# Kernel optimization log

Measured on AMD Instinct MI355X. Metric: run time of the kernel, lower is better.

Reference implementation:

```python
import jax, jax.numpy as jnp
from jax import lax
import numpy as np

C_IN, C_OUT, G, K, PAD = 64, 128, 4, 3, 1
P = K * K
CG = C_IN // G
N, H, W = 8, 64, 64
LN_EPS = 1e-6
BN_EPS = 1e-5


def setup_inputs() -> dict:
    key = jax.random.key(0)
    ks = jax.random.split(key, 32)
    r = lambda i, shape, s=0.05: jax.random.normal(ks[i], shape, dtype=jnp.float32) * s
    return dict(
        x=jax.random.normal(ks[0], (N, C_IN, H, W), dtype=jnp.float32),
        reflectance=jax.random.uniform(ks[1], (N, 1, H, W), dtype=jnp.float32),
        gain_w1=r(2, (C_IN, C_IN // 4)), gain_b1=r(3, (C_IN // 4,)),
        gain_w2=r(4, (C_IN // 4, C_IN)), gain_b2=r(5, (C_IN,)),
        tap_w=r(6, (C_IN,)), tap_b=r(7, (C_IN,)),
        dw_w=r(8, (K, K, 1, C_IN)), dw_b=r(9, (C_IN,)),
        ln_g=jnp.ones((C_IN,), jnp.float32), ln_b=jnp.zeros((C_IN,), jnp.float32),
        inp_w=r(10, (C_IN, C_IN)), inp_b=r(11, (C_IN,)),
        off_w=r(12, (C_IN, G * P * 2), 0.02), off_b=r(13, (G * P * 2,), 0.02),
        mask_w=r(14, (C_IN, G * P), 0.02), mask_b=r(15, (G * P,), 0.02),
        outp_w=r(16, (C_IN, C_IN)), outp_b=r(17, (C_IN,)),
        conv_w=r(18, (C_IN, C_OUT)), conv_b=r(19, (C_OUT,)),
        bn1_g=jnp.ones((C_IN,), jnp.float32), bn1_b=jnp.zeros((C_IN,), jnp.float32),
        bn1_m=r(20, (C_IN,)),
        bn1_v=jax.random.uniform(ks[21], (C_IN,), minval=0.5, maxval=1.5),
        bn2_g=jnp.ones((C_OUT,), jnp.float32), bn2_b=jnp.zeros((C_OUT,), jnp.float32),
        bn2_m=r(22, (C_OUT,)),
        bn2_v=jax.random.uniform(ks[23], (C_OUT,), minval=0.5, maxval=1.5),
    )


def _bilinear_gather(xg, py, px):
    # xg: (N, Hp, Wp, G, CG); py/px: (N, H, W, G, P) absolute pixel coords
    # replicates F.grid_sample(mode='bilinear', padding_mode='zeros', align_corners=False)
    n_, Hp, Wp = xg.shape[0], xg.shape[1], xg.shape[2]
    y0 = jnp.floor(py)
    x0 = jnp.floor(px)
    wy = py - y0
    wx = px - x0
    nI = jnp.arange(n_).reshape(n_, 1, 1, 1, 1)
    gI = jnp.arange(G).reshape(1, 1, 1, G, 1)
    out = jnp.zeros(py.shape + (CG,), xg.dtype)
    for dy in (0, 1):
        for dx in (0, 1):
            yi = y0 + dy
            xi = x0 + dx
            w = (wy if dy else 1.0 - wy) * (wx if dx else 1.0 - wx)
            valid = (yi >= 0) & (yi < Hp) & (xi >= 0) & (xi < Wp)
            yc = jnp.clip(yi, 0, Hp - 1).astype(jnp.int32)
            xc = jnp.clip(xi, 0, Wp - 1).astype(jnp.int32)
            v = xg[nI, yc, xc, gI]  # (N, H, W, G, P, CG)
            out = out + (w * valid.astype(w.dtype))[..., None] * v
    return out


def reference(x, reflectance, gain_w1, gain_b1, gain_w2, gain_b2, tap_w, tap_b,
              dw_w, dw_b, ln_g, ln_b, inp_w, inp_b, off_w, off_b, mask_w, mask_b,
              outp_w, outp_b, conv_w, conv_b, bn1_g, bn1_b, bn1_m, bn1_v,
              bn2_g, bn2_b, bn2_m, bn2_v):
    n_, c_, h_, w_ = x.shape
    # ---- GainBlock (SE-style): x * sigmoid(mlp(avgpool(x))) + x ----
    pooled = x.mean(axis=(2, 3))                               # (N, C)
    g = jax.nn.relu(pooled @ gain_w1 + gain_b1)
    gain = jax.nn.sigmoid(g @ gain_w2 + gain_b2)               # (N, C)
    x = x * gain[:, :, None, None] + x
    # ---- ReflectiveFeedback: x + relu(conv1x1(reflectance)) ----
    refl = jax.nn.relu(reflectance * tap_w[None, :, None, None] + tap_b[None, :, None, None])
    x = x + refl                                               # (N, C, H, W)
    # ---- DCNv3 (pytorch version, group=4, k=3, pad=1, stride=1) ----
    xh = jnp.transpose(x, (0, 2, 3, 1))                        # NHWC
    xp = xh @ inp_w + inp_b                                    # input_proj
    dw = lax.conv_general_dilated(xh, dw_w, (1, 1), 'SAME',
                                  feature_group_count=c_,
                                  dimension_numbers=('NHWC', 'HWIO', 'NHWC')) + dw_b
    mu = dw.mean(-1, keepdims=True)
    var = dw.var(-1, keepdims=True)
    dw = ln_g * (dw - mu) * lax.rsqrt(var + LN_EPS) + ln_b     # LN channels_last
    dw = jax.nn.gelu(dw, approximate=False)
    offset = (dw @ off_w + off_b).reshape(n_, h_, w_, G, P, 2)
    mask = jax.nn.softmax((dw @ mask_w + mask_b).reshape(n_, h_, w_, G, P), axis=-1)
    # dcnv3_core: pad input, build reference + dilation grids (normalized by padded size)
    xpad = jnp.pad(xp, ((0, 0), (PAD, PAD), (PAD, PAD), (0, 0)))
    Hp, Wp = h_ + 2 * PAD, w_ + 2 * PAD
    ctr = (K - 1) // 2  # = (dilation*(k-1))//2 with dilation=1
    ref_y = (jnp.arange(h_, dtype=jnp.float32) + ctr + 0.5) / Hp
    ref_x = (jnp.arange(w_, dtype=jnp.float32) + ctr + 0.5) / Wp
    kk = jnp.arange(K, dtype=jnp.float32) - ctr                # [-1, 0, 1]
    gx = jnp.repeat(kk, K) / Wp                                # w-outer, h-inner order
    gy = jnp.tile(kk, K) / Hp
    loc_x = (ref_x[None, None, :, None, None] + gx[None, None, None, None, :]
             + offset[..., 0] / Wp)                            # (N,H,W,G,P)
    loc_y = (ref_y[None, :, None, None, None] + gy[None, None, None, None, :]
             + offset[..., 1] / Hp)
    px = loc_x * Wp - 0.5   # align_corners=False pixel coords
    py = loc_y * Hp - 0.5
    xg = xpad.reshape(n_, Hp, Wp, G, CG)
    samp = _bilinear_gather(xg, py, px)                        # (N,H,W,G,P,CG)
    dcn = (samp * mask[..., None]).sum(axis=4).reshape(n_, h_, w_, c_)
    dcn = dcn @ outp_w + outp_b                                # output_proj
    y = jnp.transpose(dcn, (0, 3, 1, 2))                       # back to NCHW
    # ---- bn1 -> relu -> conv1x1 -> bn2 -> relu (eval-mode BN) ----
    y = bn1_g[None, :, None, None] * (y - bn1_m[None, :, None, None]) \
        * lax.rsqrt(bn1_v[None, :, None, None] + BN_EPS) + bn1_b[None, :, None, None]
    y = jax.nn.relu(y)
    y = jnp.einsum('nchw,cd->ndhw', y, conv_w) + conv_b[None, :, None, None]
    y = bn2_g[None, :, None, None] * (y - bn2_m[None, :, None, None]) \
        * lax.rsqrt(bn2_v[None, :, None, None] + BN_EPS) + bn2_b[None, :, None, None]
    return jax.nn.relu(y)
```

## Files before the change

kernel.cpp:

```cpp
#include <hip/hip_runtime.h>
#include <math.h>


__global__ __launch_bounds__(256) void k_pool(const float* x, float* pooled) {
    __shared__ float red[256];
    int b = blockIdx.x;
    int nc = ((b & 7) << 6) | (b >> 3);
    const float4* p4 = reinterpret_cast<const float4*>(x + (size_t)nc * 4096);
    float s = 0.f;
    for (int i = threadIdx.x; i < 1024; i += 256) {
        float4 v = p4[i];
        s += v.x + v.y + v.z + v.w;
    }
    red[threadIdx.x] = s;
    __syncthreads();
    for (int o = 128; o > 0; o >>= 1) {
        if (threadIdx.x < o) red[threadIdx.x] += red[threadIdx.x + o];
        __syncthreads();
    }
    if (threadIdx.x == 0) pooled[nc] = red[0] * (1.f / 4096.f);
}

__global__ __launch_bounds__(256) void k_xsproj(
        const float* x, const float* refl,
        const float* tap_w, const float* tap_b,
        const float* pooled,
        const float* gw1, const float* gb1,
        const float* gw2, const float* gb2,
        const float* inp_w, const float* inp_b,
        float* xs, float* xpad) {
    __shared__ float wl[64 * 64];
    __shared__ float tile[64 * 17];
    __shared__ float xsrow[16][68];
    __shared__ float hid[16];
    __shared__ float gain[64];
    __shared__ float rrow[16];
    int b = blockIdx.x;
    int n = b & 7, rem = b >> 3;
    int h = rem >> 2, wc = rem & 3, w0 = wc * 16;
    int nh = n * 64 + h;
    int tid = threadIdx.x;

    for (int i = tid; i < 1024; i += 256)
        *reinterpret_cast<float4*>(&wl[i * 4]) = reinterpret_cast<const float4*>(inp_w)[i];
    {
        int c = tid >> 2, wq = (tid & 3) * 4;
        const float4 v = *reinterpret_cast<const float4*>(
            &x[(((size_t)(n * 64 + c)) * 64 + h) * 64 + w0 + wq]);
        tile[c * 17 + wq + 0] = v.x;
        tile[c * 17 + wq + 1] = v.y;
        tile[c * 17 + wq + 2] = v.z;
        tile[c * 17 + wq + 3] = v.w;
    }
    if (tid < 16) rrow[tid] = refl[n * 4096 + h * 64 + w0 + tid];
    if (tid >= 64 && tid < 80) {
        int j = tid - 64;
        float s = gb1[j];
        for (int c = 0; c < 64; ++c) s += pooled[n * 64 + c] * gw1[c * 16 + j];
        hid[j] = fmaxf(s, 0.f);
    }
    __syncthreads();

    if (tid < 64) {
        float s = gb2[tid];
        #pragma unroll
        for (int j = 0; j < 16; ++j) s += hid[j] * gw2[j * 64 + tid];
        gain[tid] = 1.f + 1.f / (1.f + expf(-s));
    }
    __syncthreads();

    {
        int c = tid & 63, wbq = tid >> 6;
        float gv = gain[c], tw = tap_w[c], tb = tap_b[c];
        #pragma unroll
        for (int k = 0; k < 4; ++k) {
            int w = wbq + k * 4;
            float r = fmaxf(rrow[w] * tw + tb, 0.f);
            float v = tile[c * 17 + w] * gv + r;
            xsrow[w][c] = v;
            xs[(((size_t)nh) * 64 + w0 + w) * 64 + c] = v;
        }
    }
    __syncthreads();

    {
        int co = tid & 63, wg = tid >> 6;
        float acc[4];
        float bv = inp_b[co];
        #pragma unroll
        for (int i = 0; i < 4; ++i) acc[i] = bv;
        for (int c4 = 0; c4 < 64; c4 += 4) {
            float q0 = wl[(c4 + 0) * 64 + co];
            float q1 = wl[(c4 + 1) * 64 + co];
            float q2 = wl[(c4 + 2) * 64 + co];
            float q3 = wl[(c4 + 3) * 64 + co];
            #pragma unroll
            for (int i = 0; i < 4; ++i) {
                float4 d = *reinterpret_cast<const float4*>(&xsrow[wg * 4 + i][c4]);
                acc[i] += d.x * q0 + d.y * q1 + d.z * q2 + d.w * q3;
            }
        }
        const size_t rowb = (((size_t)n * 66) + (h + 1)) * 66;
        #pragma unroll
        for (int i = 0; i < 4; ++i) {
            int w = wg * 4 + i;
            xpad[(rowb + (w0 + w + 1)) * 64 + co] = acc[i];
        }
        if (wc == 0 && tid < 64) xpad[rowb * 64 + tid] = 0.f;
        if (wc == 3 && tid < 64) xpad[(rowb + 65) * 64 + tid] = 0.f;
        if (h == 0 || h == 63) {
            const size_t rb = (((size_t)n * 66) + (h == 0 ? 0 : 65)) * 66;
            for (int i = tid; i < 1024; i += 256) {
                int q = 1 + w0 + (i >> 6), cc = i & 63;
                xpad[(rb + q) * 64 + cc] = 0.f;
            }
            if (wc == 0 && tid < 64) xpad[rb * 64 + tid] = 0.f;
            if (wc == 3 && tid < 64) xpad[(rb + 65) * 64 + tid] = 0.f;
        }
    }
}

__global__ __launch_bounds__(256) void k_dwsamp(const float* xs, const float* xpad,
                       const float* dw_w, const float* dw_b,
                       const float* ln_g, const float* ln_b,
                       const float* off_w, const float* off_b,
                       const float* mask_w, const float* mask_b,
                       const float* outp_w, const float* outp_b,
                       const float* bn1_g, const float* bn1_b,
                       const float* bn1_m, const float* bn1_v,
                       float* vbuf) {
    __shared__ float  dwr[8][64];
    __shared__ float  om[8][112];
    __shared__ int4   sad[8][36];
    __shared__ float4 swt[8][36];
    __shared__ float  dcnl[8][64];

    int tid = threadIdx.x;
    int lane = tid & 63, wv = tid >> 6;
    int b = blockIdx.x;
    int n = b & 7;
    int pos = (b >> 3) * 8 + wv * 2;
    int h = pos >> 6, w0 = pos & 63;
    int pbase = n * 4096 + pos;

    {
        float dwk[9];
        #pragma unroll
        for (int k = 0; k < 9; ++k) dwk[k] = dw_w[k * 64 + lane];
        float s0 = dw_b[lane], s1 = s0;
        for (int ky = 0; ky < 3; ++ky) {
            int y = h + ky - 1;
            if (y < 0 || y > 63) continue;
            const float* xrow = xs + (((size_t)(n * 64 + y)) * 64) * 64;
            float v[4];
            #pragma unroll
            for (int dx = 0; dx < 4; ++dx) {
                int x2 = w0 - 1 + dx;
                v[dx] = (x2 >= 0 && x2 <= 63) ? xrow[x2 * 64 + lane] : 0.f;
            }
            s0 += v[0] * dwk[ky * 3 + 0] + v[1] * dwk[ky * 3 + 1] + v[2] * dwk[ky * 3 + 2];
            s1 += v[1] * dwk[ky * 3 + 0] + v[2] * dwk[ky * 3 + 1] + v[3] * dwk[ky * 3 + 2];
        }
        float lngv = ln_g[lane], lnbv = ln_b[lane];
        float ss[2] = {s0, s1};
        #pragma unroll
        for (int p = 0; p < 2; ++p) {
            float s = ss[p];
            float sum = s, sq = s * s;
            #pragma unroll
            for (int o = 32; o > 0; o >>= 1) {
                sum += __shfl_xor(sum, o, 64);
                sq  += __shfl_xor(sq,  o, 64);
            }
            float mu = sum * (1.f / 64.f);
            float var = sq * (1.f / 64.f) - mu * mu;
            float nrm = (s - mu) * rsqrtf(var + 1e-6f) * lngv + lnbv;
            dwr[wv * 2 + p][lane] = 0.5f * nrm * (1.f + erff(nrm * 0.70710678118654752f));
        }
    }
    __syncthreads();

    {
        int jb = lane * 2;
        const float* wptr;
        int stride;
        float b0 = 0.f, b1 = 0.f;
        if (lane < 36)      { wptr = off_w + jb;         stride = 72; b0 = off_b[jb];       b1 = off_b[jb + 1]; }
        else if (lane < 54) { wptr = mask_w + (jb - 72); stride = 36; b0 = mask_b[jb - 72]; b1 = mask_b[jb - 71]; }
        else                { wptr = off_w;              stride = 0; }
        float a00 = b0, a01 = b1, a10 = b0, a11 = b1;
        for (int c4 = 0; c4 < 64; c4 += 4) {
            float4 d0 = *reinterpret_cast<const float4*>(&dwr[wv * 2 + 0][c4]);
            float4 d1 = *reinterpret_cast<const float4*>(&dwr[wv * 2 + 1][c4]);
            float dk0[4] = {d0.x, d0.y, d0.z, d0.w};
            float dk1[4] = {d1.x, d1.y, d1.z, d1.w};
            #pragma unroll
            for (int k = 0; k < 4; ++k) {
                float2 w2 = *reinterpret_cast<const float2*>(wptr);
                wptr += stride;
                a00 += dk0[k] * w2.x;  a01 += dk0[k] * w2.y;
                a10 += dk1[k] * w2.x;  a11 += dk1[k] * w2.y;
            }
        }
        if (lane < 54) {
            om[wv * 2 + 0][jb] = a00;  om[wv * 2 + 0][jb + 1] = a01;
            om[wv * 2 + 1][jb] = a10;  om[wv * 2 + 1][jb + 1] = a11;
        }
    }
    __syncthreads();

    #pragma unroll
    for (int p = 0; p < 2; ++p) {
        if (lane < 36) {
            int li = wv * 2 + p;
            int g = lane / 9, pp = lane - g * 9;
            float m = om[li][72 + g * 9];
            #pragma unroll
            for (int k = 1; k < 9; ++k) m = fmaxf(m, om[li][72 + g * 9 + k]);
            float ssum = 0.f, ek = 0.f;
            #pragma unroll
            for (int k = 0; k < 9; ++k) {
                float e = expf(om[li][72 + g * 9 + k] - m);
                ssum += e;
                if (k == pp) ek = e;
            }
            float mk = ek / ssum;
            float ox = om[li][g * 18 + pp * 2];
            float oy = om[li][g * 18 + pp * 2 + 1];
            float px = (float)((w0 + p) + (pp / 3)) + ox;
            float py = (float)(h + (pp % 3)) + oy;
            float x0f = floorf(px), y0f = floorf(py);
            float wx = px - x0f, wy = py - y0f;
            int x0 = (int)x0f, y0 = (int)y0f;
            int x1 = x0 + 1, y1 = y0 + 1;
            int xc0 = min(max(x0, 0), 65), xc1 = min(max(x1, 0), 65);
            int yc0 = min(max(y0, 0), 65), yc1 = min(max(y1, 0), 65);
            float vx0 = (x0 >= 0 && x0 < 66) ? 1.f : 0.f;
            float vx1 = (x1 >= 0 && x1 < 66) ? 1.f : 0.f;
            float vy0 = (y0 >= 0 && y0 < 66) ? 1.f : 0.f;
            float vy1 = (y1 >= 0 && y1 < 66) ? 1.f : 0.f;
            float wx0 = (1.f - wx) * vx0, wx1 = wx * vx1;
            float wy0 = (1.f - wy) * vy0, wy1 = wy * vy1;
            swt[li][lane] = make_float4(mk * wy0 * wx0, mk * wy0 * wx1,
                                        mk * wy1 * wx0, mk * wy1 * wx1);
            sad[li][lane] = make_int4((yc0 * 66 + xc0) * 64, (yc0 * 66 + xc1) * 64,
                                      (yc1 * 66 + xc0) * 64, (yc1 * 66 + xc1) * 64);
        }
    }
    __syncthreads();

    {
        int gb = (lane >> 4) * 9;
        const float* xpn = xpad + (size_t)n * 66 * 66 * 64;
        #pragma unroll
        for (int p = 0; p < 2; ++p) {
            int li = wv * 2 + p;
            float acc = 0.f;
            #pragma unroll
            for (int pp = 0; pp < 9; ++pp) {
                int4   a  = sad[li][gb + pp];
                float4 cw = swt[li][gb + pp];
                acc += cw.x * xpn[a.x + lane] + cw.y * xpn[a.y + lane]
                     + cw.z * xpn[a.z + lane] + cw.w * xpn[a.w + lane];
            }
            dcnl[li][lane] = acc;
        }
    }
    __syncthreads();

    {
        float ob = outp_b[lane];
        float s0 = ob, s1 = ob;
        for (int c4 = 0; c4 < 64; c4 += 4) {
            float w0v = outp_w[(c4 + 0) * 64 + lane];
            float w1v = outp_w[(c4 + 1) * 64 + lane];
            float w2v = outp_w[(c4 + 2) * 64 + lane];
            float w3v = outp_w[(c4 + 3) * 64 + lane];
            float4 d0 = *reinterpret_cast<const float4*>(&dcnl[wv * 2 + 0][c4]);
            float4 d1 = *reinterpret_cast<const float4*>(&dcnl[wv * 2 + 1][c4]);
            s0 += d0.x * w0v + d0.y * w1v + d0.z * w2v + d0.w * w3v;
            s1 += d1.x * w0v + d1.y * w1v + d1.z * w2v + d1.w * w3v;
        }
        float sc = bn1_g[lane] * rsqrtf(bn1_v[lane] + 1e-5f);
        float sh = bn1_b[lane] - sc * bn1_m[lane];
        vbuf[(size_t)(pbase + 0) * 64 + lane] = fmaxf(sc * s0 + sh, 0.f);
        vbuf[(size_t)(pbase + 1) * 64 + lane] = fmaxf(sc * s1 + sh, 0.f);
    }
}

__global__ __launch_bounds__(256) void k_out(const float* vbuf,
                      const float* conv_w, const float* conv_b,
                      const float* bn2_g, const float* bn2_b,
                      const float* bn2_m, const float* bn2_v,
                      float* out) {
    __shared__ float vl[64 * 68];
    __shared__ float cwl[64 * 64];
    int b = blockIdx.x;
    int n = b & 7, rem = b >> 3;
    int h = rem >> 1, dh = (rem & 1) * 64;
    int tid = threadIdx.x;
    const float4* vrow4 = reinterpret_cast<const float4*>(vbuf + ((size_t)(n * 64 + h)) * 4096);
    for (int i = tid; i < 1024; i += 256) {
        int idx = i * 4;
        int w = idx >> 6, c = idx & 63;
        *reinterpret_cast<float4*>(&vl[w * 68 + c]) = vrow4[i];
    }
    for (int i = tid; i < 1024; i += 256) {
        int c = i >> 4, q = (i & 15) * 4;
        *reinterpret_cast<float4*>(&cwl[c * 64 + q]) =
            *reinterpret_cast<const float4*>(&conv_w[c * 128 + dh + q]);
    }
    __syncthreads();

    int dgrp = tid & 15, wgrp = tid >> 4;
    int dbase = dgrp * 4, wbase = wgrp * 4;
    float acc[4][4];
    #pragma unroll
    for (int i = 0; i < 4; ++i)
        #pragma unroll
        for (int j = 0; j < 4; ++j) acc[i][j] = 0.f;

    for (int c = 0; c < 64; ++c) {
        float v0 = vl[(wbase + 0) * 68 + c];
        float v1 = vl[(wbase + 1) * 68 + c];
        float v2 = vl[(wbase + 2) * 68 + c];
        float v3 = vl[(wbase + 3) * 68 + c];
        float4 wA = *reinterpret_cast<const float4*>(&cwl[c * 64 + dbase]);
        float wt[4] = {wA.x, wA.y, wA.z, wA.w};
        #pragma unroll
        for (int j = 0; j < 4; ++j) {
            acc[0][j] += v0 * wt[j];
            acc[1][j] += v1 * wt[j];
            acc[2][j] += v2 * wt[j];
            acc[3][j] += v3 * wt[j];
        }
    }

    #pragma unroll
    for (int j = 0; j < 4; ++j) {
        int d = dh + dbase + j;
        float sc = bn2_g[d] * rsqrtf(bn2_v[d] + 1e-5f);
        float sh = sc * (conv_b[d] - bn2_m[d]) + bn2_b[d];
        float4 r;
        r.x = fmaxf(sc * acc[0][j] + sh, 0.f);
        r.y = fmaxf(sc * acc[1][j] + sh, 0.f);
        r.z = fmaxf(sc * acc[2][j] + sh, 0.f);
        r.w = fmaxf(sc * acc[3][j] + sh, 0.f);
        size_t o = (((size_t)(n * 128 + d)) * 64 + h) * 64 + wbase;
        *reinterpret_cast<float4*>(out + o) = r;
    }
}

extern "C" void kernel_launch(void* const* d_in, const int* in_sizes, int n_in,
                              void* d_out, int out_size, void* d_ws, size_t ws_size,
                              hipStream_t stream) {
    const float* x      = (const float*)d_in[0];
    const float* refl   = (const float*)d_in[1];
    const float* gw1    = (const float*)d_in[2];
    const float* gb1    = (const float*)d_in[3];
    const float* gw2    = (const float*)d_in[4];
    const float* gb2    = (const float*)d_in[5];
    const float* tap_w  = (const float*)d_in[6];
    const float* tap_b  = (const float*)d_in[7];
    const float* dw_w   = (const float*)d_in[8];
    const float* dw_b   = (const float*)d_in[9];
    const float* ln_g   = (const float*)d_in[10];
    const float* ln_b   = (const float*)d_in[11];
    const float* inp_w  = (const float*)d_in[12];
    const float* inp_b  = (const float*)d_in[13];
    const float* off_w  = (const float*)d_in[14];
    const float* off_b  = (const float*)d_in[15];
    const float* mask_w = (const float*)d_in[16];
    const float* mask_b = (const float*)d_in[17];
    const float* outp_w = (const float*)d_in[18];
    const float* outp_b = (const float*)d_in[19];
    const float* conv_w = (const float*)d_in[20];
    const float* conv_b = (const float*)d_in[21];
    const float* bn1_g  = (const float*)d_in[22];
    const float* bn1_b  = (const float*)d_in[23];
    const float* bn1_m  = (const float*)d_in[24];
    const float* bn1_v  = (const float*)d_in[25];
    const float* bn2_g  = (const float*)d_in[26];
    const float* bn2_b  = (const float*)d_in[27];
    const float* bn2_m  = (const float*)d_in[28];
    const float* bn2_v  = (const float*)d_in[29];

    float* ws     = (float*)d_ws;
    float* pooled = ws;
    float* xs     = ws + 512;
    float* xpad   = xs + 2097152;
    float* vbuf   = xpad + 2230272;

    k_pool<<<512, 256, 0, stream>>>(x, pooled);
    k_xsproj<<<2048, 256, 0, stream>>>(x, refl, tap_w, tap_b, pooled,
                                       gw1, gb1, gw2, gb2, inp_w, inp_b, xs, xpad);
    k_dwsamp<<<4096, 256, 0, stream>>>(xs, xpad, dw_w, dw_b, ln_g, ln_b,
                                       off_w, off_b, mask_w, mask_b,
                                       outp_w, outp_b, bn1_g, bn1_b, bn1_m, bn1_v, vbuf);
    k_out<<<1024, 256, 0, stream>>>(vbuf, conv_w, conv_b, bn2_g, bn2_b, bn2_m, bn2_v,
                                    (float*)d_out);
}
```

Before: 211.2 us.

## Process four pixels per wave in k_dwsamp and keep offsets in registers

Each wave now handles four consecutive pixels instead of two, and blocks shrink to two waves. This amortizes the off/mask and outp_w weight loads and the depthwise row loads over more pixels. The offset logits stay in registers of the lanes that compute them and are no longer round-tripped through shared memory, so only the mask logits go through LDS. In exchange there is higher register pressure and fewer waves per block.

```diff
diff --git a/kernel.cpp b/kernel.cpp
--- a/kernel.cpp
+++ b/kernel.cpp
@@ -120,7 +120,7 @@
     }
 }
 
-__global__ __launch_bounds__(256) void k_dwsamp(const float* xs, const float* xpad,
+__global__ __launch_bounds__(128) void k_dwsamp(const float* xs, const float* xpad,
                        const float* dw_w, const float* dw_b,
                        const float* ln_g, const float* ln_b,
                        const float* off_w, const float* off_b,
@@ -130,7 +130,7 @@
                        const float* bn1_m, const float* bn1_v,
                        float* vbuf) {
     __shared__ float  dwr[8][64];
-    __shared__ float  om[8][112];
+    __shared__ float  mlog[8][40];
     __shared__ int4   sad[8][36];
     __shared__ float4 swt[8][36];
     __shared__ float  dcnl[8][64];
@@ -139,34 +139,39 @@
     int lane = tid & 63, wv = tid >> 6;
     int b = blockIdx.x;
     int n = b & 7;
-    int pos = (b >> 3) * 8 + wv * 2;
-    int h = pos >> 6, w0 = pos & 63;
-    int pbase = n * 4096 + pos;
+    int pos0 = (b >> 3) * 8 + wv * 4;
+    int h = pos0 >> 6, w0 = pos0 & 63;
+    int lbase = wv * 4;
+    int pbase = n * 4096 + pos0;
 
     {
         float dwk[9];
         #pragma unroll
         for (int k = 0; k < 9; ++k) dwk[k] = dw_w[k * 64 + lane];
-        float s0 = dw_b[lane], s1 = s0;
+        float s[4];
+        float bvv = dw_b[lane];
+        #pragma unroll
+        for (int p = 0; p < 4; ++p) s[p] = bvv;
         for (int ky = 0; ky < 3; ++ky) {
             int y = h + ky - 1;
             if (y < 0 || y > 63) continue;
-            const float* xrow = xs + (((size_t)(n * 64 + y)) * 64) * 64;
-            float v[4];
-            #pragma unroll
-            for (int dx = 0; dx < 4; ++dx) {
+            const float* xrow = xs + ((size_t)(n * 64 + y)) * 4096;
+            float v[6];
+            #pragma unroll
+            for (int dx = 0; dx < 6; ++dx) {
                 int x2 = w0 - 1 + dx;
                 v[dx] = (x2 >= 0 && x2 <= 63) ? xrow[x2 * 64 + lane] : 0.f;
             }
-            s0 += v[0] * dwk[ky * 3 + 0] + v[1] * dwk[ky * 3 + 1] + v[2] * dwk[ky * 3 + 2];
-            s1 += v[1] * dwk[ky * 3 + 0] + v[2] * dwk[ky * 3 + 1] + v[3] * dwk[ky * 3 + 2];
+            float k0 = dwk[ky * 3 + 0], k1 = dwk[ky * 3 + 1], k2 = dwk[ky * 3 + 2];
+            #pragma unroll
+            for (int p = 0; p < 4; ++p)
+                s[p] += v[p] * k0 + v[p + 1] * k1 + v[p + 2] * k2;
         }
         float lngv = ln_g[lane], lnbv = ln_b[lane];
-        float ss[2] = {s0, s1};
-        #pragma unroll
-        for (int p = 0; p < 2; ++p) {
-            float s = ss[p];
-            float sum = s, sq = s * s;
+        #pragma unroll
+        for (int p = 0; p < 4; ++p) {
+            float sv = s[p];
+            float sum = sv, sq = sv * sv;
             #pragma unroll
             for (int o = 32; o > 0; o >>= 1) {
                 sum += __shfl_xor(sum, o, 64);
@@ -174,12 +179,13 @@
             }
             float mu = sum * (1.f / 64.f);
             float var = sq * (1.f / 64.f) - mu * mu;
-            float nrm = (s - mu) * rsqrtf(var + 1e-6f) * lngv + lnbv;
-            dwr[wv * 2 + p][lane] = 0.5f * nrm * (1.f + erff(nrm * 0.70710678118654752f));
-        }
-    }
-    __syncthreads();
-
+            float nrm = (sv - mu) * rsqrtf(var + 1e-6f) * lngv + lnbv;
+            dwr[lbase + p][lane] = 0.5f * nrm * (1.f + erff(nrm * 0.70710678118654752f));
+        }
+    }
+    __syncthreads();
+
+    float a0[4], a1[4];
     {
         int jb = lane * 2;
         const float* wptr;
@@ -188,47 +194,57 @@
         if (lane < 36)      { wptr = off_w + jb;         stride = 72; b0 = off_b[jb];       b1 = off_b[jb + 1]; }
         else if (lane < 54) { wptr = mask_w + (jb - 72); stride = 36; b0 = mask_b[jb - 72]; b1 = mask_b[jb - 71]; }
         else                { wptr = off_w;              stride = 0; }
-        float a00 = b0, a01 = b1, a10 = b0, a11 = b1;
+        #pragma unroll
+        for (int p = 0; p < 4; ++p) { a0[p] = b0; a1[p] = b1; }
         for (int c4 = 0; c4 < 64; c4 += 4) {
-            float4 d0 = *reinterpret_cast<const float4*>(&dwr[wv * 2 + 0][c4]);
-            float4 d1 = *reinterpret_cast<const float4*>(&dwr[wv * 2 + 1][c4]);
+            float4 d0 = *reinterpret_cast<const float4*>(&dwr[lbase + 0][c4]);
+            float4 d1 = *reinterpret_cast<const float4*>(&dwr[lbase + 1][c4]);
+            float4 d2 = *reinterpret_cast<const float4*>(&dwr[lbase + 2][c4]);
+            float4 d3 = *reinterpret_cast<const float4*>(&dwr[lbase + 3][c4]);
             float dk0[4] = {d0.x, d0.y, d0.z, d0.w};
             float dk1[4] = {d1.x, d1.y, d1.z, d1.w};
+            float dk2[4] = {d2.x, d2.y, d2.z, d2.w};
+            float dk3[4] = {d3.x, d3.y, d3.z, d3.w};
             #pragma unroll
             for (int k = 0; k < 4; ++k) {
                 float2 w2 = *reinterpret_cast<const float2*>(wptr);
                 wptr += stride;
-                a00 += dk0[k] * w2.x;  a01 += dk0[k] * w2.y;
-                a10 += dk1[k] * w2.x;  a11 += dk1[k] * w2.y;
-            }
-        }
-        if (lane < 54) {
-            om[wv * 2 + 0][jb] = a00;  om[wv * 2 + 0][jb + 1] = a01;
-            om[wv * 2 + 1][jb] = a10;  om[wv * 2 + 1][jb + 1] = a11;
-        }
-    }
-    __syncthreads();
-
-    #pragma unroll
-    for (int p = 0; p < 2; ++p) {
-        if (lane < 36) {
-            int li = wv * 2 + p;
-            int g = lane / 9, pp = lane - g * 9;
-            float m = om[li][72 + g * 9];
-            #pragma unroll
-            for (int k = 1; k < 9; ++k) m = fmaxf(m, om[li][72 + g * 9 + k]);
+                a0[0] += dk0[k] * w2.x;  a1[0] += dk0[k] * w2.y;
+                a0[1] += dk1[k] * w2.x;  a1[1] += dk1[k] * w2.y;
+                a0[2] += dk2[k] * w2.x;  a1[2] += dk2[k] * w2.y;
+                a0[3] += dk3[k] * w2.x;  a1[3] += dk3[k] * w2.y;
+            }
+        }
+        if (lane >= 36 && lane < 54) {
+            int jm = lane * 2 - 72;
+            #pragma unroll
+            for (int p = 0; p < 4; ++p) {
+                mlog[lbase + p][jm]     = a0[p];
+                mlog[lbase + p][jm + 1] = a1[p];
+            }
+        }
+    }
+    __syncthreads();
+
+    if (lane < 36) {
+        int g = lane / 9, pp = lane - g * 9;
+        #pragma unroll
+        for (int p = 0; p < 4; ++p) {
+            int li = lbase + p;
+            const float* lrow = &mlog[li][g * 9];
+            float m = lrow[0];
+            #pragma unroll
+            for (int k = 1; k < 9; ++k) m = fmaxf(m, lrow[k]);
             float ssum = 0.f, ek = 0.f;
             #pragma unroll
             for (int k = 0; k < 9; ++k) {
-                float e = expf(om[li][72 + g * 9 + k] - m);
+                float e = expf(lrow[k] - m);
                 ssum += e;
                 if (k == pp) ek = e;
             }
             float mk = ek / ssum;
-            float ox = om[li][g * 18 + pp * 2];
-            float oy = om[li][g * 18 + pp * 2 + 1];
-            float px = (float)((w0 + p) + (pp / 3)) + ox;
-            float py = (float)(h + (pp % 3)) + oy;
+            float px = (float)((w0 + p) + (pp / 3)) + a0[p];
+            float py = (float)(h + (pp % 3)) + a1[p];
             float x0f = floorf(px), y0f = floorf(py);
             float wx = px - x0f, wy = py - y0f;
             int x0 = (int)x0f, y0 = (int)y0f;
@@ -253,8 +269,8 @@
         int gb = (lane >> 4) * 9;
         const float* xpn = xpad + (size_t)n * 66 * 66 * 64;
         #pragma unroll
-        for (int p = 0; p < 2; ++p) {
-            int li = wv * 2 + p;
+        for (int p = 0; p < 4; ++p) {
+            int li = lbase + p;
             float acc = 0.f;
             #pragma unroll
             for (int pp = 0; pp < 9; ++pp) {
@@ -270,21 +286,27 @@
 
     {
         float ob = outp_b[lane];
-        float s0 = ob, s1 = ob;
+        float s0 = ob, s1 = ob, s2 = ob, s3 = ob;
         for (int c4 = 0; c4 < 64; c4 += 4) {
             float w0v = outp_w[(c4 + 0) * 64 + lane];
             float w1v = outp_w[(c4 + 1) * 64 + lane];
             float w2v = outp_w[(c4 + 2) * 64 + lane];
             float w3v = outp_w[(c4 + 3) * 64 + lane];
-            float4 d0 = *reinterpret_cast<const float4*>(&dcnl[wv * 2 + 0][c4]);
-            float4 d1 = *reinterpret_cast<const float4*>(&dcnl[wv * 2 + 1][c4]);
+            float4 d0 = *reinterpret_cast<const float4*>(&dcnl[lbase + 0][c4]);
+            float4 d1 = *reinterpret_cast<const float4*>(&dcnl[lbase + 1][c4]);
+            float4 d2 = *reinterpret_cast<const float4*>(&dcnl[lbase + 2][c4]);
+            float4 d3 = *reinterpret_cast<const float4*>(&dcnl[lbase + 3][c4]);
             s0 += d0.x * w0v + d0.y * w1v + d0.z * w2v + d0.w * w3v;
             s1 += d1.x * w0v + d1.y * w1v + d1.z * w2v + d1.w * w3v;
+            s2 += d2.x * w0v + d2.y * w1v + d2.z * w2v + d2.w * w3v;
+            s3 += d3.x * w0v + d3.y * w1v + d3.z * w2v + d3.w * w3v;
         }
         float sc = bn1_g[lane] * rsqrtf(bn1_v[lane] + 1e-5f);
         float sh = bn1_b[lane] - sc * bn1_m[lane];
         vbuf[(size_t)(pbase + 0) * 64 + lane] = fmaxf(sc * s0 + sh, 0.f);
         vbuf[(size_t)(pbase + 1) * 64 + lane] = fmaxf(sc * s1 + sh, 0.f);
+        vbuf[(size_t)(pbase + 2) * 64 + lane] = fmaxf(sc * s2 + sh, 0.f);
+        vbuf[(size_t)(pbase + 3) * 64 + lane] = fmaxf(sc * s3 + sh, 0.f);
     }
 }
 
@@ -394,7 +416,7 @@
     k_pool<<<512, 256, 0, stream>>>(x, pooled);
     k_xsproj<<<2048, 256, 0, stream>>>(x, refl, tap_w, tap_b, pooled,
                                        gw1, gb1, gw2, gb2, inp_w, inp_b, xs, xpad);
-    k_dwsamp<<<4096, 256, 0, stream>>>(xs, xpad, dw_w, dw_b, ln_g, ln_b,
+    k_dwsamp<<<4096, 128, 0, stream>>>(xs, xpad, dw_w, dw_b, ln_g, ln_b,
                                        off_w, off_b, mask_w, mask_b,
                                        outp_w, outp_b, bn1_g, bn1_b, bn1_m, bn1_v, vbuf);
     k_out<<<1024, 256, 0, stream>>>(vbuf, conv_w, conv_b, bn2_g, bn2_b, bn2_m, bn2_v,
```

After: 200.7 us. 5.0% less time.
